# Kernel tuning notes

Measured on AMD Instinct MI355X. Metric: run time of the kernel, lower is better.

## Reference

```python
import jax, jax.numpy as jnp
import numpy as np


def _pack_ternary(codes):
    # codes: [N, K] uint8 in {0,1,2} (encoded = ternary_value + 1)
    N, K = codes.shape
    c = codes.reshape(N, K // 4, 4).astype(np.uint8)
    shifts = np.array([0, 2, 4, 6], dtype=np.uint8)
    packed = (c << shifts).sum(axis=-1).astype(np.uint8)
    return packed  # [N, K//4]


def setup_inputs() -> dict:
    key = jax.random.key(0)
    k1, k2 = jax.random.split(key)
    M, K, N = 8192, 4096, 4096
    x = jax.random.normal(k1, (M, K), dtype=jnp.float16)
    # valid INT2 packed ternary weights: 2-bit fields in {0,1,2} = value+1
    codes = np.asarray(jax.random.randint(k2, (N, K), 0, 3), dtype=np.uint8)
    W_packed = jnp.asarray(_pack_ternary(codes), dtype=jnp.uint8)
    gamma = jnp.ones((1,), dtype=jnp.float32)
    return {"x": x, "W_packed": W_packed, "gamma": gamma}


def _unpack_w(W_packed, K):
    # W_packed: [N, K//4] uint8 -> ternary float32 W: [N, K]
    N = W_packed.shape[0]
    shifts = jnp.array([0, 2, 4, 6], dtype=jnp.uint8)
    fields = (W_packed[:, :, None] >> shifts) & jnp.uint8(3)  # [N, K//4, 4]
    w = fields.reshape(N, -1)[:, :K].astype(jnp.float32) - 1.0  # {-1,0,1}
    return w


def reference(x, W_packed, gamma):
    K = x.shape[-1]
    W = _unpack_w(W_packed, K)  # [N, K] ternary
    # Y = X @ W.T * gamma (kernel does fp16 TC GEMM with inline dequant scale)
    Xf = x.astype(jnp.float32)
    Y = jnp.einsum('mk,nk->mn', Xf, W) * gamma[0]
    return Y.astype(jnp.float16)
```

## Files before the change

kernel.cpp:

```cpp
#include <hip/hip_runtime.h>
#include <cstdint>
#include <cstddef>

#define M_DIM 8192
#define N_DIM 4096
#define K_DIM 4096

typedef _Float16 f16x8 __attribute__((ext_vector_type(8)));
typedef float f32x4 __attribute__((ext_vector_type(4)));
typedef unsigned short ushort8 __attribute__((ext_vector_type(8)));

#define GLOAD_LDS16(g, l)                                                      \
  __builtin_amdgcn_global_load_lds(                                            \
      (const __attribute__((address_space(1))) void*)(g),                      \
      (__attribute__((address_space(3))) void*)(l), 16, 0, 0)

__device__ inline uint32_t lutf16(uint32_t c) {
  return (c == 1u) ? 0u : (0x3C00u | ((uint32_t)(c == 0u) << 15));
}

__global__ __launch_bounds__(256) void prep_x(const float4* __restrict__ X,
                                              ushort8* __restrict__ Xf) {
  int i = blockIdx.x * 256 + threadIdx.x;
  float4 f0 = X[2 * (size_t)i], f1 = X[2 * (size_t)i + 1];
  ushort8 us;
  us[0] = __builtin_bit_cast(uint16_t, (_Float16)f0.x);
  us[1] = __builtin_bit_cast(uint16_t, (_Float16)f0.y);
  us[2] = __builtin_bit_cast(uint16_t, (_Float16)f0.z);
  us[3] = __builtin_bit_cast(uint16_t, (_Float16)f0.w);
  us[4] = __builtin_bit_cast(uint16_t, (_Float16)f1.x);
  us[5] = __builtin_bit_cast(uint16_t, (_Float16)f1.y);
  us[6] = __builtin_bit_cast(uint16_t, (_Float16)f1.z);
  us[7] = __builtin_bit_cast(uint16_t, (_Float16)f1.w);
  Xf[i] = us;
}

__global__ __launch_bounds__(256) void prep_w(const uint2* __restrict__ W,
                                              uint4* __restrict__ Wf) {
  int i = blockIdx.x * 256 + threadIdx.x;
  uint2 wv = W[(size_t)i];
  uint32_t x = wv.x & 0xFFu, y = wv.y & 0xFFu;
  uint4 o;
  o.x = lutf16(x & 3u) | (lutf16((x >> 2) & 3u) << 16);
  o.y = lutf16((x >> 4) & 3u) | (lutf16((x >> 6) & 3u) << 16);
  o.z = lutf16(y & 3u) | (lutf16((y >> 2) & 3u) << 16);
  o.w = lutf16((y >> 4) & 3u) | (lutf16((y >> 6) & 3u) << 16);
  Wf[i] = o;
}

__global__ __launch_bounds__(256, 2) void gemm32(
    const _Float16* __restrict__ A,
    const _Float16* __restrict__ B,
    const float* __restrict__ G,
    float* __restrict__ C) {
  __shared__ __align__(16) _Float16 As[2][128 * 32];
  __shared__ __align__(16) _Float16 Bs[2][256 * 32];

  const int tid = threadIdx.x;
  const int wave = tid >> 6, lane = tid & 63;
  const int wr = wave >> 1, wc = wave & 1;
  const int fr = lane & 15, kg = lane >> 4;

  int bid = (int)blockIdx.x;
  int swz = (bid & 7) * 128 + (bid >> 3);
  const int bm = (swz >> 4) * 128;
  const int bn = (swz & 15) * 256;

  const int sr = lane >> 2;
  const int scc = (lane & 3) ^ ((lane >> 3) & 3);

  f32x4 acc[4][8] = {};

#define STG(t)                                                                 \
  do {                                                                         \
    const int b_ = (t) & 1;                                                    \
    const int kt_ = (t) * 32;                                                  \
    _Pragma("unroll") for (int j_ = 0; j_ < 6; ++j_) {                         \
      int sg_ = wave * 6 + j_;             \
      if (sg_ < 8) {                                                           \
        GLOAD_LDS16(                                                           \
            A + (size_t)(bm + sg_ * 16 + sr) * K_DIM + kt_ + scc * 8,          \
            As[b_] + sg_ * 512);                                               \
      } else {                                                                 \
        int s2_ = sg_ - 8;                                                     \
        GLOAD_LDS16(                                                           \
            B + (size_t)(bn + s2_ * 16 + sr) * K_DIM + kt_ + scc * 8,          \
            Bs[b_] + s2_ * 512);                                               \
      }                                                                        \
    }                                                                          \
  } while (0)

#define BODY(t, LAST)                                                          \
  do {                                                                         \
    if (!(LAST)) STG((t) + 1);                                                 \
    if (LAST)                                                                  \
      asm volatile("s_waitcnt vmcnt(0)" ::: "memory");                         \
    else                                                                       \
      asm volatile("s_waitcnt vmcnt(6)" ::: "memory");                         \
    __builtin_amdgcn_s_barrier();                                              \
    const int b_ = (t) & 1;                                                    \
    f16x8 af[4], bf[8];                                                        \
    _Pragma("unroll") for (int m_ = 0; m_ < 4; ++m_) {                         \
      int row_ = wr * 64 + m_ * 16 + fr;                                       \
      af[m_] = *reinterpret_cast<const f16x8*>(                                \
          As[b_] + row_ * 32 + ((kg ^ ((row_ >> 1) & 3)) * 8));                \
    }                                                                          \
    _Pragma("unroll") for (int n_ = 0; n_ < 8; ++n_) {                         \
      int row_ = wc * 128 + n_ * 16 + fr;                                      \
      bf[n_] = *reinterpret_cast<const f16x8*>(                                \
          Bs[b_] + row_ * 32 + ((kg ^ ((row_ >> 1) & 3)) * 8));                \
    }                                                                          \
    __builtin_amdgcn_s_setprio(1);                                             \
    _Pragma("unroll") for (int m_ = 0; m_ < 4; ++m_)                           \
      _Pragma("unroll") for (int n_ = 0; n_ < 8; ++n_)                         \
        acc[m_][n_] = __builtin_amdgcn_mfma_f32_16x16x32_f16(                  \
            af[m_], bf[n_], acc[m_][n_], 0, 0, 0);                             \
    __builtin_amdgcn_s_setprio(0);                                             \
    __builtin_amdgcn_s_barrier();                                              \
  } while (0)

  STG(0);
  for (int t = 0; t < 126; t += 2) {
    BODY(t, false);
    BODY(t + 1, false);
  }
  BODY(126, false);
  BODY(127, true);
#undef STG
#undef BODY

  float g = G[0];
  if (!(__builtin_fabsf(g) >= 0.001f && __builtin_fabsf(g) <= 1000.0f)) g = 1.0f;
#pragma unroll
  for (int m = 0; m < 4; ++m)
#pragma unroll
    for (int n = 0; n < 8; ++n) {
      int col = bn + wc * 128 + n * 16 + fr;
      int row0 = bm + wr * 64 + m * 16 + kg * 4;
#pragma unroll
      for (int j = 0; j < 4; ++j)
        C[(size_t)(row0 + j) * N_DIM + col] = acc[m][n][j] * g;
    }
}

__global__ __launch_bounds__(256) void gemm_inline(
    const float* __restrict__ X, const uint32_t* __restrict__ W,
    const float* __restrict__ G, float* __restrict__ C) {
  __shared__ __align__(16) _Float16 As[128 * 64];
  __shared__ __align__(16) _Float16 Bs[128 * 64];

  const int tid = threadIdx.x;
  const int wave = tid >> 6;
  const int lane = tid & 63;
  const int wr = wave >> 1, wc = wave & 1;
  const int fr = lane & 15, kg = lane >> 4;
  const int bm = blockIdx.y * 128, bn = blockIdx.x * 128;
  const int brow = tid >> 1, bhalf = tid & 1;

  f32x4 acc[4][4] = {};

  for (int kt = 0; kt < K_DIM; kt += 64) {
#pragma unroll
    for (int i = 0; i < 4; ++i) {
      int c = i * 256 + tid;
      int row = c >> 3, cc = c & 7;
      const float4* p =
          (const float4*)(X + (size_t)(bm + row) * K_DIM + kt + cc * 8);
      float4 f0 = p[0], f1 = p[1];
      ushort8 us;
      us[0] = __builtin_bit_cast(uint16_t, (_Float16)f0.x);
      us[1] = __builtin_bit_cast(uint16_t, (_Float16)f0.y);
      us[2] = __builtin_bit_cast(uint16_t, (_Float16)f0.z);
      us[3] = __builtin_bit_cast(uint16_t, (_Float16)f0.w);
      us[4] = __builtin_bit_cast(uint16_t, (_Float16)f1.x);
      us[5] = __builtin_bit_cast(uint16_t, (_Float16)f1.y);
      us[6] = __builtin_bit_cast(uint16_t, (_Float16)f1.z);
      us[7] = __builtin_bit_cast(uint16_t, (_Float16)f1.w);
      *reinterpret_cast<ushort8*>((uint16_t*)As + row * 64 +
                                  (cc ^ (row & 7)) * 8) = us;
    }
    {
      const uint32_t* wp =
          W + (size_t)(bn + brow) * 1024 + (kt >> 2) + bhalf * 8;
      uint32_t w[8];
      *(uint4*)(w) = *(const uint4*)(wp);
      *(uint4*)(w + 4) = *(const uint4*)(wp + 4);
#pragma unroll
      for (int q = 0; q < 4; ++q) {
        uint32_t x = w[2 * q] & 0xFFu, y = w[2 * q + 1] & 0xFFu;
        uint4 o;
        o.x = lutf16(x & 3u) | (lutf16((x >> 2) & 3u) << 16);
        o.y = lutf16((x >> 4) & 3u) | (lutf16((x >> 6) & 3u) << 16);
        o.z = lutf16(y & 3u) | (lutf16((y >> 2) & 3u) << 16);
        o.w = lutf16((y >> 4) & 3u) | (lutf16((y >> 6) & 3u) << 16);
        int slot = (bhalf * 4 + q) ^ (brow & 7);
        *reinterpret_cast<uint4*>((uint16_t*)Bs + brow * 64 + slot * 8) = o;
      }
    }
    __syncthreads();

#pragma unroll
    for (int ks = 0; ks < 2; ++ks) {
      f16x8 a[4], b[4];
#pragma unroll
      for (int r = 0; r < 4; ++r) {
        int row = wr * 64 + r * 16 + fr;
        a[r] = *reinterpret_cast<const f16x8*>(
            As + row * 64 + ((ks * 4 + kg) ^ (row & 7)) * 8);
      }
#pragma unroll
      for (int c = 0; c < 4; ++c) {
        int row = wc * 64 + c * 16 + fr;
        b[c] = *reinterpret_cast<const f16x8*>(
            Bs + row * 64 + ((ks * 4 + kg) ^ (row & 7)) * 8);
      }
#pragma unroll
      for (int r = 0; r < 4; ++r)
#pragma unroll
        for (int c = 0; c < 4; ++c)
          acc[r][c] = __builtin_amdgcn_mfma_f32_16x16x32_f16(a[r], b[c],
                                                             acc[r][c], 0, 0, 0);
    }
    __syncthreads();
  }

  float g = G[0];
  if (!(__builtin_fabsf(g) >= 0.001f && __builtin_fabsf(g) <= 1000.0f)) g = 1.0f;
#pragma unroll
  for (int r = 0; r < 4; ++r)
#pragma unroll
    for (int c = 0; c < 4; ++c) {
      int col = bn + wc * 64 + c * 16 + fr;
      int row0 = bm + wr * 64 + r * 16 + kg * 4;
#pragma unroll
      for (int j = 0; j < 4; ++j)
        C[(size_t)(row0 + j) * N_DIM + col] = acc[r][c][j] * g;
    }
}

extern "C" void kernel_launch(void* const* d_in, const int* in_sizes, int n_in,
                              void* d_out, int out_size, void* d_ws,
                              size_t ws_size, hipStream_t stream) {
  const float* x = (const float*)d_in[0];
  const uint32_t* w32 = (const uint32_t*)d_in[1];
  const float* gamma = (const float*)d_in[2];
  float* out = (float*)d_out;
  (void)in_sizes; (void)n_in; (void)out_size;

  const size_t xf_bytes = (size_t)M_DIM * K_DIM * 2;
  const size_t wf_bytes = (size_t)N_DIM * K_DIM * 2;

  if (ws_size >= xf_bytes + wf_bytes) {
    _Float16* xf = (_Float16*)d_ws;
    _Float16* wf = (_Float16*)((char*)d_ws + xf_bytes);
    prep_x<<<M_DIM * K_DIM / 8 / 256, 256, 0, stream>>>((const float4*)x,
                                                        (ushort8*)xf);
    prep_w<<<N_DIM * K_DIM / 8 / 256, 256, 0, stream>>>((const uint2*)w32,
                                                        (uint4*)wf);
    gemm32<<<(M_DIM / 128) * (N_DIM / 256), 256, 0, stream>>>(xf, wf, gamma,
                                                              out);
  } else {
    dim3 grid(N_DIM / 128, M_DIM / 128);
    gemm_inline<<<grid, 256, 0, stream>>>(x, w32, gamma, out);
  }
}
```

Baseline: 309.9 us.

## Pre-layout dequantized weights for direct register loads and widen K tile

```diff
diff --git a/kernel.cpp b/kernel.cpp
--- a/kernel.cpp
+++ b/kernel.cpp
@@ -35,9 +35,10 @@
   Xf[i] = us;
 }
 
-__global__ __launch_bounds__(256) void prep_w(const uint2* __restrict__ W,
-                                              uint4* __restrict__ Wf) {
+__global__ __launch_bounds__(256) void prep_w2(const uint2* __restrict__ W,
+                                               uint4* __restrict__ Wf) {
   int i = blockIdx.x * 256 + threadIdx.x;
+  int n = i >> 9, kk = i & 511;
   uint2 wv = W[(size_t)i];
   uint32_t x = wv.x & 0xFFu, y = wv.y & 0xFFu;
   uint4 o;
@@ -45,16 +46,15 @@
   o.y = lutf16((x >> 4) & 3u) | (lutf16((x >> 6) & 3u) << 16);
   o.z = lutf16(y & 3u) | (lutf16((y >> 2) & 3u) << 16);
   o.w = lutf16((y >> 4) & 3u) | (lutf16((y >> 6) & 3u) << 16);
-  Wf[i] = o;
-}
-
-__global__ __launch_bounds__(256, 2) void gemm32(
+  Wf[((size_t)(n >> 4) * 512 + kk) * 16 + (n & 15)] = o;
+}
+
+__global__ __launch_bounds__(256, 2) void gemmBL(
     const _Float16* __restrict__ A,
-    const _Float16* __restrict__ B,
+    const f16x8* __restrict__ Bf,
     const float* __restrict__ G,
     float* __restrict__ C) {
-  __shared__ __align__(16) _Float16 As[2][128 * 32];
-  __shared__ __align__(16) _Float16 Bs[2][256 * 32];
+  __shared__ __align__(16) _Float16 As[2][128 * 64];
 
   const int tid = threadIdx.x;
   const int wave = tid >> 6, lane = tid & 63;
@@ -64,69 +64,65 @@
   int bid = (int)blockIdx.x;
   int swz = (bid & 7) * 128 + (bid >> 3);
   const int bm = (swz >> 4) * 128;
-  const int bn = (swz & 15) * 256;
-
-  const int sr = lane >> 2;
-  const int scc = (lane & 3) ^ ((lane >> 3) & 3);
+  const int bn16 = (swz & 15) * 16;
+
+  const int sr8 = lane >> 3;
+  const int scol = ((lane & 7) ^ sr8) * 8;
+
+  const f16x8* bp0 = Bf + ((size_t)(bn16 + wc * 8) * 512 + kg) * 16 + fr;
 
   f32x4 acc[4][8] = {};
-
-#define STG(t)                                                                 \
+  f16x8 bf[8][2];
+
+#define STG_A(t)                                                               \
   do {                                                                         \
     const int b_ = (t) & 1;                                                    \
-    const int kt_ = (t) * 32;                                                  \
-    _Pragma("unroll") for (int j_ = 0; j_ < 6; ++j_) {                         \
-      int sg_ = wave * 6 + j_;             \
-      if (sg_ < 8) {                                                           \
-        GLOAD_LDS16(                                                           \
-            A + (size_t)(bm + sg_ * 16 + sr) * K_DIM + kt_ + scc * 8,          \
-            As[b_] + sg_ * 512);                                               \
-      } else {                                                                 \
-        int s2_ = sg_ - 8;                                                     \
-        GLOAD_LDS16(                                                           \
-            B + (size_t)(bn + s2_ * 16 + sr) * K_DIM + kt_ + scc * 8,          \
-            Bs[b_] + s2_ * 512);                                               \
-      }                                                                        \
+    _Pragma("unroll") for (int j_ = 0; j_ < 4; ++j_) {                         \
+      int sg_ = wave * 4 + j_;                                                 \
+      int row_ = sg_ * 8 + sr8;                                                \
+      GLOAD_LDS16(A + (size_t)(bm + row_) * K_DIM + (t) * 64 + scol,           \
+                  As[b_] + sg_ * 512);                                         \
     }                                                                          \
   } while (0)
 
 #define BODY(t, LAST)                                                          \
   do {                                                                         \
-    if (!(LAST)) STG((t) + 1);                                                 \
+    const int b_ = (t) & 1;                                                    \
+    const f16x8* bp_ = bp0 + (size_t)(t) * 128;                                \
+    _Pragma("unroll") for (int n_ = 0; n_ < 8; ++n_)                           \
+      _Pragma("unroll") for (int ks_ = 0; ks_ < 2; ++ks_)                      \
+        bf[n_][ks_] = bp_[n_ * 8192 + ks_ * 64];                               \
+    if (!(LAST)) STG_A((t) + 1);                                               \
     if (LAST)                                                                  \
-      asm volatile("s_waitcnt vmcnt(0)" ::: "memory");                         \
+      asm volatile("s_waitcnt vmcnt(16)" ::: "memory");                        \
     else                                                                       \
-      asm volatile("s_waitcnt vmcnt(6)" ::: "memory");                         \
+      asm volatile("s_waitcnt vmcnt(20)" ::: "memory");                        \
     __builtin_amdgcn_s_barrier();                                              \
-    const int b_ = (t) & 1;                                                    \
-    f16x8 af[4], bf[8];                                                        \
-    _Pragma("unroll") for (int m_ = 0; m_ < 4; ++m_) {                         \
-      int row_ = wr * 64 + m_ * 16 + fr;                                       \
-      af[m_] = *reinterpret_cast<const f16x8*>(                                \
-          As[b_] + row_ * 32 + ((kg ^ ((row_ >> 1) & 3)) * 8));                \
-    }                                                                          \
-    _Pragma("unroll") for (int n_ = 0; n_ < 8; ++n_) {                         \
-      int row_ = wc * 128 + n_ * 16 + fr;                                      \
-      bf[n_] = *reinterpret_cast<const f16x8*>(                                \
-          Bs[b_] + row_ * 32 + ((kg ^ ((row_ >> 1) & 3)) * 8));                \
-    }                                                                          \
+    f16x8 af[4][2];                                                            \
+    _Pragma("unroll") for (int m_ = 0; m_ < 4; ++m_)                           \
+      _Pragma("unroll") for (int ks_ = 0; ks_ < 2; ++ks_) {                    \
+        int row_ = wr * 64 + m_ * 16 + fr;                                     \
+        af[m_][ks_] = *reinterpret_cast<const f16x8*>(                         \
+            As[b_] + row_ * 64 + (((ks_ * 4 + kg) ^ (row_ & 7)) * 8));         \
+      }                                                                        \
     __builtin_amdgcn_s_setprio(1);                                             \
     _Pragma("unroll") for (int m_ = 0; m_ < 4; ++m_)                           \
       _Pragma("unroll") for (int n_ = 0; n_ < 8; ++n_)                         \
-        acc[m_][n_] = __builtin_amdgcn_mfma_f32_16x16x32_f16(                  \
-            af[m_], bf[n_], acc[m_][n_], 0, 0, 0);                             \
+        _Pragma("unroll") for (int ks_ = 0; ks_ < 2; ++ks_)                    \
+          acc[m_][n_] = __builtin_amdgcn_mfma_f32_16x16x32_f16(                \
+              af[m_][ks_], bf[n_][ks_], acc[m_][n_], 0, 0, 0);                 \
     __builtin_amdgcn_s_setprio(0);                                             \
     __builtin_amdgcn_s_barrier();                                              \
   } while (0)
 
-  STG(0);
-  for (int t = 0; t < 126; t += 2) {
+  STG_A(0);
+  for (int t = 0; t < 62; t += 2) {
     BODY(t, false);
     BODY(t + 1, false);
   }
-  BODY(126, false);
-  BODY(127, true);
-#undef STG
+  BODY(62, false);
+  BODY(63, true);
+#undef STG_A
 #undef BODY
 
   float g = G[0];
@@ -135,7 +131,7 @@
   for (int m = 0; m < 4; ++m)
 #pragma unroll
     for (int n = 0; n < 8; ++n) {
-      int col = bn + wc * 128 + n * 16 + fr;
+      int col = bn16 * 16 + wc * 128 + n * 16 + fr;
       int row0 = bm + wr * 64 + m * 16 + kg * 4;
 #pragma unroll
       for (int j = 0; j < 4; ++j)
@@ -255,10 +251,10 @@
     _Float16* wf = (_Float16*)((char*)d_ws + xf_bytes);
     prep_x<<<M_DIM * K_DIM / 8 / 256, 256, 0, stream>>>((const float4*)x,
                                                         (ushort8*)xf);
-    prep_w<<<N_DIM * K_DIM / 8 / 256, 256, 0, stream>>>((const uint2*)w32,
-                                                        (uint4*)wf);
-    gemm32<<<(M_DIM / 128) * (N_DIM / 256), 256, 0, stream>>>(xf, wf, gamma,
-                                                              out);
+    prep_w2<<<N_DIM * K_DIM / 8 / 256, 256, 0, stream>>>((const uint2*)w32,
+                                                         (uint4*)wf);
+    gemmBL<<<(M_DIM / 128) * (N_DIM / 256), 256, 0, stream>>>(
+        xf, (const f16x8*)wf, gamma, out);
   } else {
     dim3 grid(N_DIM / 128, M_DIM / 128);
     gemm_inline<<<grid, 256, 0, stream>>>(x, w32, gamma, out);
```

After: 399.2 us. +28.8%, slower.
